# Performance work log

Measured on AMD Instinct MI355X. Metric: run time of the kernel, lower is better.

Reference implementation:

```python
import jax, jax.numpy as jnp
import numpy as np

B, S, D, H = 4, 2048, 1024, 16
DEPTH = D // H


def setup_inputs() -> dict:
    key = jax.random.key(0)
    ks = jax.random.split(key, 12)
    inp = {
        'v': jax.random.normal(ks[0], (B, S, D), dtype=jnp.float32),
        'k': jax.random.normal(ks[1], (B, S, D), dtype=jnp.float32),
        'q': jax.random.normal(ks[2], (B, S, D), dtype=jnp.float32),
        # key-padding mask: 1.0 = masked position, 0.0 = attend
        'mask': jax.random.randint(ks[3], (B, 1, 1, S), 0, 2).astype(jnp.float32),
        'Wq': jax.random.normal(ks[4], (D, D), dtype=jnp.float32) / np.sqrt(D),
        'bq': jnp.zeros((D,), dtype=jnp.float32),
        'Wk': jax.random.normal(ks[5], (D, D), dtype=jnp.float32) / np.sqrt(D),
        'bk': jnp.zeros((D,), dtype=jnp.float32),
        'Wv': jax.random.normal(ks[6], (D, D), dtype=jnp.float32) / np.sqrt(D),
        'bv': jnp.zeros((D,), dtype=jnp.float32),
        'Wo': jax.random.normal(ks[7], (D, D), dtype=jnp.float32) / np.sqrt(D),
        'bo': jnp.zeros((D,), dtype=jnp.float32),
    }
    return inp


def _split_heads(x):
    # [B, S, D] -> [B, H, S, depth]
    b, s, _ = x.shape
    return x.reshape(b, s, H, DEPTH).transpose(0, 2, 1, 3)


def reference(v, k, q, mask, Wq, bq, Wk, bk, Wv, bv, Wo, bo):
    qh = _split_heads(q @ Wq + bq)  # [B,H,S,depth]
    kh = _split_heads(k @ Wk + bk)
    vh = _split_heads(v @ Wv + bv)
    logits = jnp.einsum('bhqd,bhkd->bhqk', qh, kh) / jnp.sqrt(
        jnp.asarray(DEPTH, dtype=qh.dtype))
    logits = logits + mask * (-1e9)
    attn = jax.nn.softmax(logits, axis=-1)  # [B,H,Sq,Sk]
    out = jnp.einsum('bhqk,bhkd->bhqd', attn, vh)
    out = out.transpose(0, 2, 1, 3).reshape(q.shape[0], -1, D)  # [B,S,D]
    return out @ Wo + bo
```

## Files before the change

kernel.cpp:

```cpp
#include <hip/hip_runtime.h>
#include <hip/hip_bf16.h>
#include <stdint.h>


#define S_LEN 2048
#define NHEAD 16
#define DEPTH 64
#define DMODEL 1024

typedef __bf16 bf16x8 __attribute__((ext_vector_type(8)));
typedef float f32x4 __attribute__((ext_vector_type(4)));
typedef uint16_t u16x8 __attribute__((ext_vector_type(8)));
typedef uint16_t u16x4 __attribute__((ext_vector_type(4)));

#if __has_builtin(__builtin_amdgcn_exp2f)
#define EXP2F(x) __builtin_amdgcn_exp2f(x)
#else
#define EXP2F(x) __builtin_exp2f(x)
#endif

__device__ __forceinline__ uint16_t f2bf(float x) {
    __hip_bfloat16 h = __float2bfloat16(x);
    union { __hip_bfloat16 h; uint16_t u; } v; v.h = h; return v.u;
}
__device__ __forceinline__ u16x8 pack8(f32x4 a, f32x4 b) {
    u16x8 r;
#pragma unroll
    for (int i = 0; i < 4; ++i) { r[i] = f2bf(a[i]); r[i + 4] = f2bf(b[i]); }
    return r;
}
__device__ __forceinline__ u16x8 cvt8(const float* p) {
    f32x4 lo = *(const f32x4*)p, hi = *(const f32x4*)(p + 4);
    return pack8(lo, hi);
}
__device__ __forceinline__ void async16(const void* g, void* l) {
    __builtin_amdgcn_global_load_lds((__attribute__((address_space(1))) void*)(g),
                                     (__attribute__((address_space(3))) void*)(l),
                                     16, 0, 0);
}

__global__ void mask_scan(const float* __restrict__ mask, int* __restrict__ gidx,
                          int* __restrict__ nb) {
    __shared__ int part[256];
    const int b = blockIdx.x, tid = threadIdx.x;
    int flags[8], cnt = 0;
#pragma unroll
    for (int i = 0; i < 8; ++i) {
        flags[i] = (mask[b * S_LEN + tid * 8 + i] == 0.0f) ? 1 : 0;
        cnt += flags[i];
    }
    part[tid] = cnt;
    __syncthreads();
    for (int st = 1; st < 256; st <<= 1) {
        int v = (tid >= st) ? part[tid - st] : 0;
        __syncthreads();
        part[tid] += v;
        __syncthreads();
    }
    int run = part[tid] - cnt;
#pragma unroll
    for (int i = 0; i < 8; ++i) {
        if (flags[i]) { gidx[b * S_LEN + run] = tid * 8 + i; ++run; }
    }
    if (tid == 255) nb[b] = part[255];
}

__global__ void transpose4(const float* __restrict__ w0, const float* __restrict__ w1,
                           const float* __restrict__ w2, const float* __restrict__ w3,
                           uint16_t* __restrict__ dst) {
    __shared__ uint16_t tile[32][33];
    const float* src = (blockIdx.z == 0) ? w0 : (blockIdx.z == 1) ? w1
                     : (blockIdx.z == 2) ? w2 : w3;
    uint16_t* d = dst + (size_t)blockIdx.z * DMODEL * DMODEL;
    int bx = blockIdx.x * 32, by = blockIdx.y * 32;
    int x = threadIdx.x, y0 = threadIdx.y;
#pragma unroll
    for (int i = 0; i < 4; ++i) {
        int y = y0 + i * 8;
        tile[y][x] = f2bf(src[(size_t)(by + y) * DMODEL + bx + x]);
    }
    __syncthreads();
#pragma unroll
    for (int i = 0; i < 4; ++i) {
        int y = y0 + i * 8;
        d[(size_t)(bx + y) * DMODEL + by + x] = tile[x][y];
    }
}

__global__ void cast2(const float* __restrict__ a, const float* __restrict__ b,
                      uint16_t* __restrict__ da, uint16_t* __restrict__ db) {
    const float* src = blockIdx.y ? b : a;
    uint16_t* dst = blockIdx.y ? db : da;
    size_t i = ((size_t)blockIdx.x * 256 + threadIdx.x) * 8;
    *(u16x8*)(dst + i) = cvt8(src + i);
}

__global__ void zero_tails(const int* __restrict__ nb, uint16_t* __restrict__ Kc,
                           uint16_t* __restrict__ Vc) {
    const int bh = blockIdx.x, b = bh >> 4, t = threadIdx.x;
    const int nbv = nb[b];
    const int end = ((nbv + 63) >> 6) << 6;
    const int tail = end - nbv;
    for (int i = t; i < tail * 64; i += 256) {
        int r = nbv + (i >> 6), c = i & 63;
        Kc[((size_t)bh * S_LEN + r) * DEPTH + c] = 0;
    }
    for (int i = t; i < tail * 64; i += 256) {
        int s = nbv + (i >> 6), d = i & 63;
        int off = s & 63;
        int c1 = ((off & 15) << 2) | (off >> 4);
        int c2 = ((((c1 >> 3) ^ (d & 7)) & 7) << 3) | (c1 & 7);
        Vc[((size_t)bh * DEPTH + d) * S_LEN + (s & ~63) + c2] = 0;
    }
}

__global__ __launch_bounds__(256, 3)
void qkv_gemm(const uint16_t* __restrict__ qb, const uint16_t* __restrict__ kb,
              const float* __restrict__ vf, const uint16_t* __restrict__ WT4,
              const float* __restrict__ bq, const float* __restrict__ bk,
              const float* __restrict__ bv, uint16_t* __restrict__ Qh,
              uint16_t* __restrict__ Kc, uint16_t* __restrict__ Vc,
              const int* __restrict__ gidx, const int* __restrict__ nb, int zbase) {
    const int z = zbase + blockIdx.z;
    const int fid = blockIdx.x + 8 * blockIdx.y;
    const int n0 = ((fid >> 3) & 7) * 128;
    const int m0 = ((((fid >> 6) << 3)) | (fid & 7)) * 128;
    const int b_ = m0 >> 11;
    int nbv = 0x7FFFFFFF;
    if (z >= 1) {
        nbv = nb[b_];
        if ((m0 & 2047) >= nbv) return;
    }

    __shared__ __align__(16) uint16_t As[2][128 * 32];
    __shared__ __align__(16) uint16_t Bs[2][128 * 32];

    const int t = threadIdx.x;
    const int lane = t & 63, quad = lane >> 4, l16 = lane & 15;
    const int w = t >> 6, wm = w >> 1, wn = w & 1;
    const int K = DMODEL;

    const int r_ld = lane >> 2;
    const int c_ld = (lane & 3) * 8;
    const uint16_t* gB = WT4 + (size_t)z * DMODEL * DMODEL + (size_t)(n0 + r_ld) * K + c_ld;
    const float* bias = (z == 0) ? bq : (z == 1) ? bk : bv;

    const uint16_t* pA0 = nullptr;
    const uint16_t* pA1 = nullptr;
    const float* pAa = nullptr;
    const float* pAb = nullptr;
    if (z == 0) {
        pA0 = qb + (size_t)(m0 + (w * 2 + 0) * 16 + r_ld) * K + c_ld;
        pA1 = pA0 + (size_t)16 * K;
    } else if (z == 1) {
        int sp0 = (m0 & 2047) + (w * 2 + 0) * 16 + r_ld;
        int sp1 = sp0 + 16;
        int r0 = (sp0 < nbv) ? gidx[(b_ << 11) + sp0] : 0;
        int r1 = (sp1 < nbv) ? gidx[(b_ << 11) + sp1] : 0;
        pA0 = kb + ((size_t)(b_ << 11) + r0) * K + c_ld;
        pA1 = kb + ((size_t)(b_ << 11) + r1) * K + c_ld;
    } else {
        int spa = (m0 & 2047) + (t >> 2);
        int spb = spa + 64;
        int ra = (spa < nbv) ? gidx[(b_ << 11) + spa] : 0;
        int rb = (spb < nbv) ? gidx[(b_ << 11) + spb] : 0;
        pAa = vf + ((size_t)(b_ << 11) + ra) * K + (t & 3) * 8;
        pAb = vf + ((size_t)(b_ << 11) + rb) * K + (t & 3) * 8;
    }

    f32x4 acc[4][4];
    const f32x4 z4 = {0.f, 0.f, 0.f, 0.f};
#pragma unroll
    for (int mt = 0; mt < 4; ++mt)
#pragma unroll
        for (int nt = 0; nt < 4; ++nt) acc[mt][nt] = z4;

    f32x4 frA[4], frB[4];

#define STAGEB(KC, BUF) do {                                                   \
        async16(gB + (size_t)((w * 2 + 0) * 16) * K + (KC), &Bs[(BUF)][(w * 2 + 0) * 512]); \
        async16(gB + (size_t)((w * 2 + 1) * 16) * K + (KC), &Bs[(BUF)][(w * 2 + 1) * 512]); \
    } while (0)
#define STAGEA(KC, BUF) do {                                                   \
        async16(pA0 + (KC), &As[(BUF)][(w * 2 + 0) * 512]);                    \
        async16(pA1 + (KC), &As[(BUF)][(w * 2 + 1) * 512]);                    \
    } while (0)
#define LOADA2(KC, FR) do {                                                    \
        FR[0] = *(const f32x4*)(pAa + (KC));                                   \
        FR[1] = *(const f32x4*)(pAa + (KC) + 4);                               \
        FR[2] = *(const f32x4*)(pAb + (KC));                                   \
        FR[3] = *(const f32x4*)(pAb + (KC) + 4);                               \
    } while (0)
#define WRITEA2(BUF, FR) do {                                                  \
        uint16_t* d_ = &As[(BUF)][0] + t * 8;                                  \
        *(u16x8*)d_ = pack8(FR[0], FR[1]);                                     \
        *(u16x8*)(d_ + 2048) = pack8(FR[2], FR[3]);                            \
    } while (0)
#define COMPUTE(BUF) do {                                                      \
        bf16x8 af[4], bfr[4];                                                  \
        _Pragma("unroll")                                                      \
        for (int mt = 0; mt < 4; ++mt)                                         \
            af[mt] = *(const bf16x8*)&As[(BUF)][(wm * 64 + mt * 16 + l16) * 32 + quad * 8]; \
        _Pragma("unroll")                                                      \
        for (int nt = 0; nt < 4; ++nt)                                         \
            bfr[nt] = *(const bf16x8*)&Bs[(BUF)][(wn * 64 + nt * 16 + l16) * 32 + quad * 8]; \
        __builtin_amdgcn_s_setprio(1);                                         \
        _Pragma("unroll")                                                      \
        for (int mt = 0; mt < 4; ++mt)                                         \
            _Pragma("unroll")                                                  \
            for (int nt = 0; nt < 4; ++nt)                                     \
                acc[mt][nt] = __builtin_amdgcn_mfma_f32_16x16x32_bf16(af[mt], bfr[nt], \
                                                                      acc[mt][nt], 0, 0, 0); \
        __builtin_amdgcn_s_setprio(0);                                         \
    } while (0)

    STAGEB(0, 0);
    if (z <= 1) { STAGEA(0, 0); }
    else { LOADA2(0, frA); WRITEA2(0, frA); LOADA2(32, frA); }
    __syncthreads();

    for (int s = 0; s < 32; s += 2) {
        if (s + 1 < 32) { STAGEB((s + 1) * 32, 1); if (z <= 1) STAGEA((s + 1) * 32, 1); }
        if (z == 2 && s + 2 < 32) LOADA2((s + 2) * 32, frB);
        COMPUTE(0);
        if (z == 2 && s + 1 < 32) WRITEA2(1, frA);
        __syncthreads();
        if (s + 2 < 32) { STAGEB((s + 2) * 32, 0); if (z <= 1) STAGEA((s + 2) * 32, 0); }
        if (z == 2 && s + 3 < 32) LOADA2((s + 3) * 32, frA);
        COMPUTE(1);
        if (z == 2 && s + 2 < 32) WRITEA2(0, frB);
        __syncthreads();
    }
#undef STAGEB
#undef STAGEA
#undef LOADA2
#undef WRITEA2
#undef COMPUTE

#pragma unroll
    for (int nt = 0; nt < 4; ++nt) {
        int col = n0 + wn * 64 + nt * 16 + l16;
        float bval = bias[col];
        int h = col >> 6, dp = col & 63;
#pragma unroll
        for (int mt = 0; mt < 4; ++mt) {
#pragma unroll
            for (int r = 0; r < 4; ++r) {
                int row = m0 + wm * 64 + mt * 16 + quad * 4 + r;
                float val = acc[mt][nt][r] + bval;
                int b = row >> 11, s = row & 2047;
                if (z == 0) {
                    Qh[(((size_t)(b * NHEAD + h)) * S_LEN + s) * DEPTH + dp] = f2bf(val);
                } else if (z == 1) {
                    if (s < nbv) {
                        int c2 = ((((dp >> 3) ^ (s & 7)) & 7) << 3) | (dp & 7);
                        Kc[(((size_t)(b * NHEAD + h)) * S_LEN + s) * DEPTH + c2] = f2bf(val);
                    }
                } else {
                    if (s < nbv) {
                        int off = s & 63;
                        int c1 = ((off & 15) << 2) | (off >> 4);
                        int c2 = ((((c1 >> 3) ^ (dp & 7)) & 7) << 3) | (c1 & 7);
                        Vc[(((size_t)(b * NHEAD + h)) * DEPTH + dp) * S_LEN
                           + (s & ~63) + c2] = f2bf(val);
                    }
                }
            }
        }
    }
}

__global__ __launch_bounds__(256, 3)
void out_gemm(const uint16_t* __restrict__ ctx, const uint16_t* __restrict__ Wt,
              const float* __restrict__ bias, float* __restrict__ outp) {
    const int fid = blockIdx.x + 8 * blockIdx.y;
    const int n0 = ((fid >> 3) & 7) * 128;
    const int m0 = ((((fid >> 6) << 3)) | (fid & 7)) * 128;

    __shared__ __align__(16) uint16_t As[2][128 * 32];
    __shared__ __align__(16) uint16_t Bs[2][128 * 32];

    const int t = threadIdx.x;
    const int lane = t & 63, quad = lane >> 4, l16 = lane & 15;
    const int w = t >> 6, wm = w >> 1, wn = w & 1;
    const int K = DMODEL;

    const int r_ld = lane >> 2;
    const int c_ld = (lane & 3) * 8;
    const uint16_t* gB = Wt + (size_t)(n0 + r_ld) * K + c_ld;

    int row0 = m0 + (w * 2 + 0) * 16 + r_ld;
    int row1 = row0 + 16;
    const uint16_t* pA0 = ctx + ((size_t)((row0 >> 11) * NHEAD) * S_LEN + (row0 & 2047)) * DEPTH + c_ld;
    const uint16_t* pA1 = ctx + ((size_t)((row1 >> 11) * NHEAD) * S_LEN + (row1 & 2047)) * DEPTH + c_ld;

    auto stage = [&](int kc, int buf) {
        async16(gB + (size_t)((w * 2 + 0) * 16) * K + kc, &Bs[buf][(w * 2 + 0) * 512]);
        async16(gB + (size_t)((w * 2 + 1) * 16) * K + kc, &Bs[buf][(w * 2 + 1) * 512]);
        size_t aoff = ((size_t)(kc >> 6) << 17) + (kc & 63);
        async16(pA0 + aoff, &As[buf][(w * 2 + 0) * 512]);
        async16(pA1 + aoff, &As[buf][(w * 2 + 1) * 512]);
    };

    f32x4 acc[4][4];
    const f32x4 z4 = {0.f, 0.f, 0.f, 0.f};
#pragma unroll
    for (int mt = 0; mt < 4; ++mt)
#pragma unroll
        for (int nt = 0; nt < 4; ++nt) acc[mt][nt] = z4;

    stage(0, 0);
    __syncthreads();

    for (int s = 0; s < 32; ++s) {
        const int cb = s & 1;
        if (s + 1 < 32) stage((s + 1) * 32, cb ^ 1);
        {
            bf16x8 af[4], bfr[4];
#pragma unroll
            for (int mt = 0; mt < 4; ++mt)
                af[mt] = *(const bf16x8*)&As[cb][(wm * 64 + mt * 16 + l16) * 32 + quad * 8];
#pragma unroll
            for (int nt = 0; nt < 4; ++nt)
                bfr[nt] = *(const bf16x8*)&Bs[cb][(wn * 64 + nt * 16 + l16) * 32 + quad * 8];
            __builtin_amdgcn_s_setprio(1);
#pragma unroll
            for (int mt = 0; mt < 4; ++mt)
#pragma unroll
                for (int nt = 0; nt < 4; ++nt)
                    acc[mt][nt] = __builtin_amdgcn_mfma_f32_16x16x32_bf16(af[mt], bfr[nt],
                                                                          acc[mt][nt], 0, 0, 0);
            __builtin_amdgcn_s_setprio(0);
        }
        __syncthreads();
    }

#pragma unroll
    for (int nt = 0; nt < 4; ++nt) {
        int col = n0 + wn * 64 + nt * 16 + l16;
        float bval = bias[col];
#pragma unroll
        for (int mt = 0; mt < 4; ++mt) {
#pragma unroll
            for (int r = 0; r < 4; ++r) {
                int row = m0 + wm * 64 + mt * 16 + quad * 4 + r;
                outp[(size_t)row * DMODEL + col] = acc[mt][nt][r] + bval;
            }
        }
    }
}

__global__ __launch_bounds__(256, 3)
void flash_attn(const uint16_t* __restrict__ Qh, const uint16_t* __restrict__ Kc,
                const uint16_t* __restrict__ Vc, const int* __restrict__ nb,
                uint16_t* __restrict__ ctx) {
    __shared__ __align__(16) uint16_t Ks[2][64 * 64];
    __shared__ __align__(16) uint16_t Vs[2][64 * 64];
    __shared__ __align__(16) uint16_t Ps[4][16 * 72];

    const int t = threadIdx.x;
    const int w = t >> 6, lane = t & 63, quad = lane >> 4, l16 = lane & 15;
    const int fid = blockIdx.x + 16 * blockIdx.y;
    const int q0 = ((fid >> 3) & 15) * 128;
    const int bh = ((fid >> 7) << 3) | (fid & 7);
    const int b = bh >> 4;
    const int nbv = nb[b];
    const int ntiles = (nbv + 63) >> 6;

    const int srow8 = lane >> 3, scol8 = (lane & 7) * 8;
    const uint16_t* pKn = Kc + ((size_t)bh * S_LEN + w * 16 + srow8) * DEPTH + scol8;
    const uint16_t* pVn = Vc + ((size_t)bh * DEPTH + w * 16 + srow8) * S_LEN + scol8;
    uint16_t* dK0 = &Ks[0][w * 16 * 64];
    uint16_t* dK1 = &Ks[1][w * 16 * 64];
    uint16_t* dV0 = &Vs[0][w * 16 * 64];
    uint16_t* dV1 = &Vs[1][w * 16 * 64];

    bf16x8 aq[2][2];
#pragma unroll
    for (int mt = 0; mt < 2; ++mt)
#pragma unroll
        for (int kc = 0; kc < 2; ++kc)
            aq[mt][kc] = *(const bf16x8*)(Qh + ((size_t)bh * S_LEN + q0 + w * 32 + mt * 16 + l16) * DEPTH
                                          + kc * 32 + quad * 8);

    float lrow[2][4];
    f32x4 Oacc[2][4];
    const f32x4 z4 = {0.f, 0.f, 0.f, 0.f};
#pragma unroll
    for (int mt = 0; mt < 2; ++mt)
#pragma unroll
        for (int r = 0; r < 4; ++r) lrow[mt][r] = 0.f;
#pragma unroll
    for (int mt = 0; mt < 2; ++mt)
#pragma unroll
        for (int nt = 0; nt < 4; ++nt) Oacc[mt][nt] = z4;

    const float C2 = 0.18033688f;
    const float M2 = 17.312340f;
    const int swzk = l16 & 7;

    async16(pKn, dK0); async16(pKn + 8 * DEPTH, dK0 + 8 * 64);
    async16(pVn, dV0); async16(pVn + 8 * S_LEN, dV0 + 8 * 64);
    pKn += 64 * DEPTH; pVn += 64;
    __syncthreads();

    for (int kt = 0; kt < ntiles; ++kt) {
        const int cur = kt & 1;
        if (kt + 1 < ntiles) {
            uint16_t* dK = cur ? dK0 : dK1;
            uint16_t* dV = cur ? dV0 : dV1;
            async16(pKn, dK); async16(pKn + 8 * DEPTH, dK + 8 * 64);
            async16(pVn, dV); async16(pVn + 8 * S_LEN, dV + 8 * 64);
            pKn += 64 * DEPTH; pVn += 64;
        }
        const uint16_t* ksrc = cur ? &Ks[1][0] : &Ks[0][0];
        const uint16_t* vsrc = cur ? &Vs[1][0] : &Vs[0][0];
        const int k0 = kt * 64;

        float pen[4];
#pragma unroll
        for (int nt = 0; nt < 4; ++nt)
            pen[nt] = (k0 + nt * 16 + l16 < nbv) ? -M2 : -2e9f;

        f32x4 sacc[2][4];
#pragma unroll
        for (int mt = 0; mt < 2; ++mt)
#pragma unroll
            for (int nt = 0; nt < 4; ++nt) sacc[mt][nt] = z4;
        __builtin_amdgcn_s_setprio(1);
#pragma unroll
        for (int kc = 0; kc < 2; ++kc) {
#pragma unroll
            for (int nt = 0; nt < 4; ++nt) {
                bf16x8 bk = *(const bf16x8*)&ksrc[(nt * 16 + l16) * 64 + (((kc * 4 + quad) ^ swzk) << 3)];
#pragma unroll
                for (int mt = 0; mt < 2; ++mt)
                    sacc[mt][nt] = __builtin_amdgcn_mfma_f32_16x16x32_bf16(aq[mt][kc], bk,
                                                                           sacc[mt][nt], 0, 0, 0);
            }
        }
        __builtin_amdgcn_s_setprio(0);

        bf16x8 bvr[2][4];
#pragma unroll
        for (int kc = 0; kc < 2; ++kc)
#pragma unroll
            for (int nt = 0; nt < 4; ++nt)
                bvr[kc][nt] = *(const bf16x8*)&vsrc[(nt * 16 + l16) * 64 + (((kc * 4 + quad) ^ swzk) << 3)];

#pragma unroll
        for (int mt = 0; mt < 2; ++mt) {
#pragma unroll
            for (int r = 0; r < 4; ++r) {
                float p0 = EXP2F(fmaf(sacc[mt][0][r], C2, pen[0]));
                float p1 = EXP2F(fmaf(sacc[mt][1][r], C2, pen[1]));
                float p2 = EXP2F(fmaf(sacc[mt][2][r], C2, pen[2]));
                float p3 = EXP2F(fmaf(sacc[mt][3][r], C2, pen[3]));
                lrow[mt][r] += (p0 + p1) + (p2 + p3);
                u16x4 pk;
                pk[0] = f2bf(p0); pk[1] = f2bf(p1); pk[2] = f2bf(p2); pk[3] = f2bf(p3);
                *(u16x4*)&Ps[w][(quad * 4 + r) * 72 + l16 * 4] = pk;
            }
            __builtin_amdgcn_s_setprio(1);
#pragma unroll
            for (int kc = 0; kc < 2; ++kc) {
                bf16x8 ap = *(const bf16x8*)&Ps[w][l16 * 72 + kc * 32 + quad * 8];
#pragma unroll
                for (int nt = 0; nt < 4; ++nt)
                    Oacc[mt][nt] = __builtin_amdgcn_mfma_f32_16x16x32_bf16(ap, bvr[kc][nt],
                                                                           Oacc[mt][nt], 0, 0, 0);
            }
            __builtin_amdgcn_s_setprio(0);
        }
        __syncthreads();
    }

#pragma unroll
    for (int mt = 0; mt < 2; ++mt) {
#pragma unroll
        for (int r = 0; r < 4; ++r) {
            float rs = lrow[mt][r];
            rs += __shfl_xor(rs, 1);
            rs += __shfl_xor(rs, 2);
            rs += __shfl_xor(rs, 4);
            rs += __shfl_xor(rs, 8);
            float inv = 1.0f / rs;
            int srow = q0 + w * 32 + mt * 16 + quad * 4 + r;
            size_t base = ((size_t)bh * S_LEN + srow) * DEPTH;
#pragma unroll
            for (int nt = 0; nt < 4; ++nt)
                ctx[base + nt * 16 + l16] = f2bf(Oacc[mt][nt][r] * inv);
        }
    }
}

extern "C" void kernel_launch(void* const* d_in, const int* in_sizes, int n_in,
                              void* d_out, int out_size, void* d_ws, size_t ws_size,
                              hipStream_t stream) {
    const float* v    = (const float*)d_in[0];
    const float* k    = (const float*)d_in[1];
    const float* q    = (const float*)d_in[2];
    const float* mask = (const float*)d_in[3];
    const float* Wq   = (const float*)d_in[4];
    const float* bq   = (const float*)d_in[5];
    const float* Wk   = (const float*)d_in[6];
    const float* bk   = (const float*)d_in[7];
    const float* Wv   = (const float*)d_in[8];
    const float* bv   = (const float*)d_in[9];
    const float* Wo   = (const float*)d_in[10];
    const float* bo   = (const float*)d_in[11];

    char* p = (char*)d_ws;
    uint16_t* WT4 = (uint16_t*)p; p += (size_t)4 * DMODEL * DMODEL * 2;
    uint16_t* Qh  = (uint16_t*)p; p += (size_t)64 * S_LEN * DEPTH * 2;
    int* gidx     = (int*)p;      p += (size_t)4 * S_LEN * 4;
    int* nb       = (int*)p;      p += 16;
    size_t used = (size_t)(p - (char*)d_ws);
    const size_t half16 = (size_t)8192 * DMODEL * 2;

    const bool bigws = (ws_size >= used + 2 * half16);
    uint16_t *qb, *kb, *Kc, *Vc;
    if (bigws) {
        qb = (uint16_t*)((char*)d_ws + used);
        kb = qb + (size_t)8192 * DMODEL;
        Kc = (uint16_t*)d_out;
        Vc = Kc + (size_t)64 * S_LEN * DEPTH;
    } else {
        qb = (uint16_t*)d_out;
        kb = qb + (size_t)8192 * DMODEL;
        Kc = qb;
        Vc = kb;
    }

    mask_scan<<<4, 256, 0, stream>>>(mask, gidx, nb);
    transpose4<<<dim3(32, 32, 4), dim3(32, 8), 0, stream>>>(Wq, Wk, Wv, Wo, WT4);
    cast2<<<dim3(4096, 2), 256, 0, stream>>>(q, k, qb, kb);

    if (bigws) {
        qkv_gemm<<<dim3(8, 64, 3), 256, 0, stream>>>(qb, kb, v, WT4, bq, bk, bv,
                                                     Qh, Kc, Vc, gidx, nb, 0);
    } else {
        qkv_gemm<<<dim3(8, 64, 1), 256, 0, stream>>>(qb, kb, v, WT4, bq, bk, bv,
                                                     Qh, Kc, Vc, gidx, nb, 0);
        qkv_gemm<<<dim3(8, 64, 1), 256, 0, stream>>>(qb, kb, v, WT4, bq, bk, bv,
                                                     Qh, Kc, Vc, gidx, nb, 1);
        qkv_gemm<<<dim3(8, 64, 1), 256, 0, stream>>>(qb, kb, v, WT4, bq, bk, bv,
                                                     Qh, Kc, Vc, gidx, nb, 2);
    }
    zero_tails<<<64, 256, 0, stream>>>(nb, Kc, Vc);

    flash_attn<<<dim3(16, 64), 256, 0, stream>>>(Qh, Kc, Vc, nb, Qh );

    out_gemm<<<dim3(8, 64), 256, 0, stream>>>(Qh, WT4 + (size_t)3 * DMODEL * DMODEL,
                                              bo, (float*)d_out);
}
```

Measured before the change: 335.3 us.

## Stage V-projection epilogue through LDS for coalesced transposed stores; drop double buffering

For the V projection, the epilogue now writes the bf16 results into a swizzled shared-memory tile and then emits 16-byte coalesced stores of the transposed V layout. The previous path did scattered 2-byte global stores. The main K loop is also simplified from a double-buffered, register-prefetched pipeline to a single-buffered load/sync/compute/sync loop, since the shared buffer is enlarged to 32KB and reused for the epilogue. This exposes global load latency in the main loop, which reduces overlap. It also writes the tail rows beyond nbv for V, which were previously skipped.

```diff
diff --git a/kernel.cpp b/kernel.cpp
--- a/kernel.cpp
+++ b/kernel.cpp
@@ -132,8 +132,9 @@
         if ((m0 & 2047) >= nbv) return;
     }
 
-    __shared__ __align__(16) uint16_t As[2][128 * 32];
-    __shared__ __align__(16) uint16_t Bs[2][128 * 32];
+    __shared__ __align__(16) uint16_t SH[128 * 128];
+    uint16_t* As = SH;
+    uint16_t* Bs = SH + 128 * 32;
 
     const int t = threadIdx.x;
     const int lane = t & 63, quad = lane >> 4, l16 = lane & 15;
@@ -175,67 +176,72 @@
 #pragma unroll
         for (int nt = 0; nt < 4; ++nt) acc[mt][nt] = z4;
 
-    f32x4 frA[4], frB[4];
-
-#define STAGEB(KC, BUF) do {                                                   \
-        async16(gB + (size_t)((w * 2 + 0) * 16) * K + (KC), &Bs[(BUF)][(w * 2 + 0) * 512]); \
-        async16(gB + (size_t)((w * 2 + 1) * 16) * K + (KC), &Bs[(BUF)][(w * 2 + 1) * 512]); \
-    } while (0)
-#define STAGEA(KC, BUF) do {                                                   \
-        async16(pA0 + (KC), &As[(BUF)][(w * 2 + 0) * 512]);                    \
-        async16(pA1 + (KC), &As[(BUF)][(w * 2 + 1) * 512]);                    \
-    } while (0)
-#define LOADA2(KC, FR) do {                                                    \
-        FR[0] = *(const f32x4*)(pAa + (KC));                                   \
-        FR[1] = *(const f32x4*)(pAa + (KC) + 4);                               \
-        FR[2] = *(const f32x4*)(pAb + (KC));                                   \
-        FR[3] = *(const f32x4*)(pAb + (KC) + 4);                               \
-    } while (0)
-#define WRITEA2(BUF, FR) do {                                                  \
-        uint16_t* d_ = &As[(BUF)][0] + t * 8;                                  \
-        *(u16x8*)d_ = pack8(FR[0], FR[1]);                                     \
-        *(u16x8*)(d_ + 2048) = pack8(FR[2], FR[3]);                            \
-    } while (0)
-#define COMPUTE(BUF) do {                                                      \
-        bf16x8 af[4], bfr[4];                                                  \
-        _Pragma("unroll")                                                      \
-        for (int mt = 0; mt < 4; ++mt)                                         \
-            af[mt] = *(const bf16x8*)&As[(BUF)][(wm * 64 + mt * 16 + l16) * 32 + quad * 8]; \
-        _Pragma("unroll")                                                      \
-        for (int nt = 0; nt < 4; ++nt)                                         \
-            bfr[nt] = *(const bf16x8*)&Bs[(BUF)][(wn * 64 + nt * 16 + l16) * 32 + quad * 8]; \
-        __builtin_amdgcn_s_setprio(1);                                         \
-        _Pragma("unroll")                                                      \
-        for (int mt = 0; mt < 4; ++mt)                                         \
-            _Pragma("unroll")                                                  \
-            for (int nt = 0; nt < 4; ++nt)                                     \
-                acc[mt][nt] = __builtin_amdgcn_mfma_f32_16x16x32_bf16(af[mt], bfr[nt], \
-                                                                      acc[mt][nt], 0, 0, 0); \
-        __builtin_amdgcn_s_setprio(0);                                         \
-    } while (0)
-
-    STAGEB(0, 0);
-    if (z <= 1) { STAGEA(0, 0); }
-    else { LOADA2(0, frA); WRITEA2(0, frA); LOADA2(32, frA); }
-    __syncthreads();
-
-    for (int s = 0; s < 32; s += 2) {
-        if (s + 1 < 32) { STAGEB((s + 1) * 32, 1); if (z <= 1) STAGEA((s + 1) * 32, 1); }
-        if (z == 2 && s + 2 < 32) LOADA2((s + 2) * 32, frB);
-        COMPUTE(0);
-        if (z == 2 && s + 1 < 32) WRITEA2(1, frA);
-        __syncthreads();
-        if (s + 2 < 32) { STAGEB((s + 2) * 32, 0); if (z <= 1) STAGEA((s + 2) * 32, 0); }
-        if (z == 2 && s + 3 < 32) LOADA2((s + 3) * 32, frA);
-        COMPUTE(1);
-        if (z == 2 && s + 2 < 32) WRITEA2(0, frB);
-        __syncthreads();
-    }
-#undef STAGEB
-#undef STAGEA
-#undef LOADA2
-#undef WRITEA2
-#undef COMPUTE
+    for (int kc = 0; kc < K; kc += 32) {
+        async16(gB + (size_t)((w * 2 + 0) * 16) * K + kc, &Bs[(w * 2 + 0) * 512]);
+        async16(gB + (size_t)((w * 2 + 1) * 16) * K + kc, &Bs[(w * 2 + 1) * 512]);
+        if (z <= 1) {
+            async16(pA0 + kc, &As[(w * 2 + 0) * 512]);
+            async16(pA1 + kc, &As[(w * 2 + 1) * 512]);
+        } else {
+            f32x4 a0 = *(const f32x4*)(pAa + kc), a1 = *(const f32x4*)(pAa + kc + 4);
+            f32x4 b0 = *(const f32x4*)(pAb + kc), b1 = *(const f32x4*)(pAb + kc + 4);
+            uint16_t* d_ = As + t * 8;
+            *(u16x8*)d_ = pack8(a0, a1);
+            *(u16x8*)(d_ + 2048) = pack8(b0, b1);
+        }
+        __syncthreads();
+
+        bf16x8 af[4], bfr[4];
+#pragma unroll
+        for (int mt = 0; mt < 4; ++mt)
+            af[mt] = *(const bf16x8*)&As[(wm * 64 + mt * 16 + l16) * 32 + quad * 8];
+#pragma unroll
+        for (int nt = 0; nt < 4; ++nt)
+            bfr[nt] = *(const bf16x8*)&Bs[(wn * 64 + nt * 16 + l16) * 32 + quad * 8];
+#pragma unroll
+        for (int mt = 0; mt < 4; ++mt)
+#pragma unroll
+            for (int nt = 0; nt < 4; ++nt)
+                acc[mt][nt] = __builtin_amdgcn_mfma_f32_16x16x32_bf16(af[mt], bfr[nt],
+                                                                      acc[mt][nt], 0, 0, 0);
+        __syncthreads();
+    }
+
+    if (z == 2) {
+#pragma unroll
+        for (int nt = 0; nt < 4; ++nt) {
+            int c = wn * 64 + nt * 16 + l16;
+            float bval = bias[n0 + c];
+            int dp = (n0 + c) & 63;
+            int key = (c & 15) << 4;
+            char* rowp = (char*)SH + c * 256;
+#pragma unroll
+            for (int mt = 0; mt < 4; ++mt) {
+#pragma unroll
+                for (int r = 0; r < 4; ++r) {
+                    int rowl = wm * 64 + mt * 16 + quad * 4 + r;
+                    int off = rowl & 63, half = rowl >> 6;
+                    int c1 = ((off & 15) << 2) | (off >> 4);
+                    int c2 = ((((c1 >> 3) ^ (dp & 7)) & 7) << 3) | (c1 & 7);
+                    int j = half * 128 + c2 * 2;
+                    *(uint16_t*)(rowp + (j ^ key)) = f2bf(acc[mt][nt][r] + bval);
+                }
+            }
+        }
+        __syncthreads();
+        const int sloc = m0 & 2047;
+#pragma unroll
+        for (int p = 0; p < 8; ++p) {
+            int task = p * 256 + t;
+            int c = task >> 4, g = task & 15;
+            int colg = n0 + c, h = colg >> 6, dp = colg & 63;
+            u16x8 vdat = *(const u16x8*)((const char*)SH + c * 256
+                                         + ((g * 16) ^ ((c & 15) << 4)));
+            size_t elem = ((size_t)(b_ * NHEAD + h) * DEPTH + dp) * S_LEN + sloc + g * 8;
+            *(u16x8*)(Vc + elem) = vdat;
+        }
+        return;
+    }
 
 #pragma unroll
     for (int nt = 0; nt < 4; ++nt) {
@@ -251,18 +257,10 @@
                 int b = row >> 11, s = row & 2047;
                 if (z == 0) {
                     Qh[(((size_t)(b * NHEAD + h)) * S_LEN + s) * DEPTH + dp] = f2bf(val);
-                } else if (z == 1) {
+                } else {
                     if (s < nbv) {
                         int c2 = ((((dp >> 3) ^ (s & 7)) & 7) << 3) | (dp & 7);
                         Kc[(((size_t)(b * NHEAD + h)) * S_LEN + s) * DEPTH + c2] = f2bf(val);
-                    }
-                } else {
-                    if (s < nbv) {
-                        int off = s & 63;
-                        int c1 = ((off & 15) << 2) | (off >> 4);
-                        int c2 = ((((c1 >> 3) ^ (dp & 7)) & 7) << 3) | (c1 & 7);
-                        Vc[(((size_t)(b * NHEAD + h)) * DEPTH + dp) * S_LEN
-                           + (s & ~63) + c2] = f2bf(val);
                     }
                 }
             }
```

After: 328.1 us. 1.02x faster.
